# Kernel optimization log

Hardware: AMD Instinct MI355X
Metric: run time of the kernel (lower is better)

## Reference

```python
import jax, jax.numpy as jnp
import numpy as np

DILATIONS = (1, 2, 4, 8, 16, 32)
T_ENC = 168   # encoder context length
T_PRED = 24   # predict_sequence_length
FILTERS = 64
FEAT = 15
HIDDEN = 128
B = 2048


def setup_inputs() -> dict:
    key = jax.random.key(0)
    ks = jax.random.split(key, 12)
    w = lambda k, s: jax.random.normal(k, s, jnp.float32) * 0.05
    return {
        "decoder_features": jax.random.normal(ks[0], (B, T_PRED, FEAT), jnp.float32),
        "decoder_init_input": jax.random.normal(ks[1], (B, 1), jnp.float32),
        "encoder_outputs": jax.random.normal(ks[2], (len(DILATIONS), B, T_ENC, FILTERS), jnp.float32),
        "W1": w(ks[3], (FEAT + 1, FILTERS)), "b1": jnp.zeros((FILTERS,), jnp.float32),
        "W2": w(ks[4], (FILTERS, 2 * FILTERS)), "b2": jnp.zeros((2 * FILTERS,), jnp.float32),
        "W3": w(ks[5], (FILTERS, 2 * FILTERS)),
        "W4": w(ks[6], (FILTERS, 2 * FILTERS)), "b4": jnp.zeros((2 * FILTERS,), jnp.float32),
        "W5": w(ks[7], (FILTERS * len(DILATIONS), HIDDEN)), "b5": jnp.zeros((HIDDEN,), jnp.float32),
        "W6": w(ks[8], (HIDDEN, 1)), "b6": jnp.zeros((1,), jnp.float32),
    }


def reference(decoder_features, decoder_init_input, encoder_outputs,
              W1, b1, W2, b2, W3, W4, b4, W5, b5, W6, b6):
    L, Bd, Te, F = encoder_outputs.shape
    # Preallocated growing state buffer (the torch/keras code does tf.concat each step)
    bufs0 = jnp.concatenate(
        [encoder_outputs, jnp.zeros((L, Bd, T_PRED, F), encoder_outputs.dtype)], axis=2)

    def step(bufs, t):
        # Note: the source never updates prev_output, so (eval mode) this_input
        # always uses decoder_init_input concatenated with step-t features.
        this_input = jnp.concatenate(
            [decoder_init_input, decoder_features[:, t]], axis=-1)  # [B, FEAT+1]
        x = jnp.tanh(this_input @ W1 + b1)  # [B, F]
        skips_all = []
        for l, d in enumerate(DILATIONS):
            # encoder_outputs[l][:, -d, :] of a buffer of current length T_ENC + t
            state = jax.lax.dynamic_index_in_dim(
                bufs[l], T_ENC + t - d, axis=1, keepdims=False)  # [B, F]
            dc = state @ W2 + b2 + x @ W3  # [B, 2F]
            f, g = jnp.split(dc, 2, axis=1)
            gated = jnp.tanh(f) * jax.nn.sigmoid(g)  # [B, F]
            out = gated @ W4 + b4  # [B, 2F]
            skips, res = jnp.split(out, 2, axis=1)
            x = x + res
            bufs = bufs.at[l, :, T_ENC + t, :].set(x)
            skips_all.append(skips)
        sk = jax.nn.relu(jnp.concatenate(skips_all, axis=1))  # [B, F*L]
        h = jax.nn.relu(sk @ W5 + b5)  # [B, HIDDEN]
        y = h @ W6 + b6  # [B, 1]
        return bufs, y

    _, ys = jax.lax.scan(step, bufs0, jnp.arange(T_PRED))
    return jnp.transpose(ys, (1, 0, 2))  # [B, T_PRED, 1]
```

## Files before the change

kernel.cpp:

```cpp
#include <hip/hip_runtime.h>
#include <hip/hip_bf16.h>
#include <cstddef>

#define NB 2048
#define TENC 168
#define TPRED 24

typedef _Float16 h8 __attribute__((ext_vector_type(8)));
typedef float f4v __attribute__((ext_vector_type(4)));

#define LBAR() asm volatile("s_waitcnt lgkmcnt(0)\ns_barrier" ::: "memory")

__device__ __forceinline__ float tanh_fast(float v) {
  v = fminf(v, 15.0f);
  const float ex = __expf(2.0f * v);
  return (ex - 1.0f) * __builtin_amdgcn_rcpf(ex + 1.0f);
}
__device__ __forceinline__ float sig_fast(float v) {
  return __builtin_amdgcn_rcpf(1.0f + __expf(-v));
}

#define MFMA16(a, b, c) __builtin_amdgcn_mfma_f32_16x16x32_f16((a), (b), (c), 0, 0, 0)

__global__ __launch_bounds__(512, 1) void dec_phase1(
    const float* __restrict__ feat,
    const float* __restrict__ dinit,
    const float* __restrict__ enc,
    const float* __restrict__ W1,
    const float* __restrict__ b1,
    const float* __restrict__ W2,
    const float* __restrict__ b2,
    const float* __restrict__ W3,
    const float* __restrict__ W4,
    const float* __restrict__ b4,
    _Float16* __restrict__ skbuf,
    int t_steps)
{
  __shared__ _Float16 ring[23][16][72];
  __shared__ _Float16 g16v[2][16][72];
  __shared__ _Float16 xf16[16][72];
  __shared__ float    xf32[64][20];
  __shared__ _Float16 W43h[64][136];

  const int tid = threadIdx.x;
  const int w   = tid >> 6;
  const int ln  = tid & 63;
  const int i   = ln & 15;
  const int q   = ln >> 4;
  const int q8  = q * 8;
  const int e0  = blockIdx.x * 16;

  float* W3s  = (float*)&ring[0][0][0];
  float* W4rs = W3s + 64 * 128;
  for (int idx = tid; idx < 2048; idx += 512)
    ((float4*)W3s)[idx] = ((const float4*)W3)[idx];
  for (int idx = tid; idx < 1024; idx += 512) {
    const int row = idx >> 4, seg = idx & 15;
    *(float4*)&W4rs[row * 64 + seg * 4] = *(const float4*)&W4[row * 128 + 64 + seg * 4];
  }
  __syncthreads();
  {
    const int c = tid & 127, k0 = (tid >> 7) << 4;
    float acc[16];
    #pragma unroll
    for (int r = 0; r < 16; ++r) acc[r] = 0.0f;
    for (int m = 0; m < 64; ++m) {
      const float w3v = W3s[m * 128 + c];
      #pragma unroll
      for (int r = 0; r < 16; ++r) acc[r] += W4rs[(k0 + r) * 64 + m] * w3v;
    }
    #pragma unroll
    for (int r = 0; r < 16; ++r) W43h[k0 + r][c] = (_Float16)acc[r];
  }
  __syncthreads();

  const int fs = w & 3;
  const int cf = 16 * fs + i;
  const int cg = 64 + cf;
  const int cs = 16 * (w - 4) + i;

  h8 BW2f[2], BW2g[2], BW3f[2], BW3g[2], B43f[2], B43g[2], B4s[2], B4r[2];
  float b2f = 0.f, b2g = 0.f, b4s_b = 0.f, b4r_b = 0.f;
  if (w < 4) {
    #pragma unroll
    for (int kk = 0; kk < 2; ++kk)
      #pragma unroll
      for (int j = 0; j < 8; ++j) {
        const int k = kk * 32 + q8 + j;
        BW2f[kk][j] = (_Float16)W2[k * 128 + cf];
        BW2g[kk][j] = (_Float16)W2[k * 128 + cg];
        BW3f[kk][j] = (_Float16)W3[k * 128 + cf];
        BW3g[kk][j] = (_Float16)W3[k * 128 + cg];
        B43f[kk][j] = W43h[k][cf];
        B43g[kk][j] = W43h[k][cg];
      }
    b2f = b2[cf]; b2g = b2[cg];
  } else {
    #pragma unroll
    for (int kk = 0; kk < 2; ++kk)
      #pragma unroll
      for (int j = 0; j < 8; ++j) {
        const int k = kk * 32 + q8 + j;
        B4s[kk][j] = (_Float16)W4[k * 128 + cs];
        B4r[kk][j] = (_Float16)W4[k * 128 + 64 + cs];
      }
    b4s_b = b4[cs]; b4r_b = b4[64 + cs];
  }
  float w1r[16];
  #pragma unroll
  for (int ii = 0; ii < 16; ++ii) w1r[ii] = W1[ii * 64 + ln];
  const float b1r  = b1[ln];
  const float ini0 = dinit[e0 + 2 * w];
  const float ini1 = dinit[e0 + 2 * w + 1];

  for (int idx = tid; idx < 1920; idx += 512) {
    const int c = idx & 7, el = (idx >> 3) & 15, s = idx >> 7;
    int l, j;
    if (s == 0)      { l = 0; j = 0; }
    else if (s < 3)  { l = 1; j = s - 1; }
    else if (s < 7)  { l = 2; j = s - 3; }
    else             { l = 3; j = s - 7; }
    const int d = 1 << l;
    const float* ep = enc + (((size_t)l * NB + e0 + el) * TENC + (TENC + j - d)) * 64 + c * 8;
    h8 hv;
    #pragma unroll
    for (int u = 0; u < 8; ++u) hv[u] = (_Float16)ep[u];
    *(h8*)&ring[s][el][c * 8] = hv;
  }

  #pragma unroll
  for (int s = 0; s < 2; ++s) {
    const int el = 2 * w + s;
    const float* fp = feat + (size_t)(e0 + el) * TPRED * 15;
    float u = b1r + (s ? ini1 : ini0) * w1r[0];
    #pragma unroll
    for (int ii = 0; ii < 15; ++ii) u += fp[ii] * w1r[ii + 1];
    const float xv = tanh_fast(u);
    xf16[el][ln] = (_Float16)xv;
    xf32[ln][el] = xv;
  }
  LBAR();

  f4v Zf = {0,0,0,0}, Zg = {0,0,0,0}, xreg = {0,0,0,0};

  for (int t = 0; t < t_steps; ++t) {
    const int tn = (t + 1 < t_steps) ? t + 1 : t;
    f4v pfa[2], pfb[2], pfc[2];
    float2 pfd[2]; float pfe[2];
    #pragma unroll
    for (int s = 0; s < 2; ++s) {
      const float* fp = feat + ((size_t)(e0 + 2 * w + s) * TPRED + tn) * 15;
      pfa[s] = *(const f4v*)(fp);
      pfb[s] = *(const f4v*)(fp + 4);
      pfc[s] = *(const f4v*)(fp + 8);
      pfd[s] = *(const float2*)(fp + 12);
      pfe[s] = fp[14];
    }

    h8 s0a[4], s1a[4], s4a0, s4a1;
    f4v p4[4], p5[4];
    if (w < 4) {
      const int t4 = (t < 16) ? t : 0;
      const float* e4 = enc + (((size_t)4 * NB + e0 + i) * TENC + (152 + t4)) * 64 + q8;
      const float* e5 = enc + (((size_t)5 * NB + e0 + i) * TENC + (136 + t )) * 64 + q8;
      p4[0] = *(const f4v*)(e4);      p4[1] = *(const f4v*)(e4 + 4);
      p4[2] = *(const f4v*)(e4 + 32); p4[3] = *(const f4v*)(e4 + 36);
      p5[0] = *(const f4v*)(e5);      p5[1] = *(const f4v*)(e5 + 4);
      p5[2] = *(const f4v*)(e5 + 32); p5[3] = *(const f4v*)(e5 + 36);

      #pragma unroll
      for (int l = 0; l < 4; ++l) {
        const int d = 1 << l;
        const int slot = (d - 1) + (t & (d - 1));
        s0a[l] = *(const h8*)&ring[slot][i][q8];
        s1a[l] = *(const h8*)&ring[slot][i][32 + q8];
      }
      {
        const int slot4 = 15 + (t & 7);
        s4a0 = *(const h8*)&ring[slot4][i][q8];
        s4a1 = *(const h8*)&ring[slot4][i][32 + q8];
      }

      const h8 a2 = *(const h8*)&xf16[i][q8];
      const h8 a3 = *(const h8*)&xf16[i][32 + q8];
      Zf = (f4v){0,0,0,0};  Zg = (f4v){0,0,0,0};
      Zf = MFMA16(a2, BW3f[0], Zf); Zf = MFMA16(a3, BW3f[1], Zf);
      Zg = MFMA16(a2, BW3g[0], Zg); Zg = MFMA16(a3, BW3g[1], Zg);

      f4v dcf = Zf, dcg = Zg;
      dcf = MFMA16(s0a[0], BW2f[0], dcf); dcf = MFMA16(s1a[0], BW2f[1], dcf);
      dcg = MFMA16(s0a[0], BW2g[0], dcg); dcg = MFMA16(s1a[0], BW2g[1], dcg);
      #pragma unroll
      for (int r = 0; r < 4; ++r) {
        const float gd = tanh_fast(dcf[r] + b2f) * sig_fast(dcg[r] + b2g);
        g16v[0][4 * q + r][cf] = (_Float16)gd;
      }
    } else {
      xreg = *(const f4v*)&xf32[cs][4 * q];
    }
    LBAR();

    #pragma unroll
    for (int l = 1; l < 6; ++l) {
      const int pm1 = (l - 1) & 1;
      const h8 gA0 = *(const h8*)&g16v[pm1][i][q8];
      const h8 gA1 = *(const h8*)&g16v[pm1][i][32 + q8];

      if (w < 4) {
        Zf = MFMA16(gA0, B43f[0], Zf); Zf = MFMA16(gA1, B43f[1], Zf);
        Zg = MFMA16(gA0, B43g[0], Zg); Zg = MFMA16(gA1, B43g[1], Zg);
        h8 sa0, sa1;
        if (l <= 3) { sa0 = s0a[l]; sa1 = s1a[l]; }
        else if (l == 4) {
          if (t < 16) {
            #pragma unroll
            for (int u = 0; u < 4; ++u) {
              sa0[u] = (_Float16)p4[0][u]; sa0[u + 4] = (_Float16)p4[1][u];
              sa1[u] = (_Float16)p4[2][u]; sa1[u + 4] = (_Float16)p4[3][u];
            }
          } else { sa0 = s4a0; sa1 = s4a1; }
        } else {
          #pragma unroll
          for (int u = 0; u < 4; ++u) {
            sa0[u] = (_Float16)p5[0][u]; sa0[u + 4] = (_Float16)p5[1][u];
            sa1[u] = (_Float16)p5[2][u]; sa1[u + 4] = (_Float16)p5[3][u];
          }
        }
        f4v dcf = Zf, dcg = Zg;
        dcf = MFMA16(sa0, BW2f[0], dcf); dcf = MFMA16(sa1, BW2f[1], dcf);
        dcg = MFMA16(sa0, BW2g[0], dcg); dcg = MFMA16(sa1, BW2g[1], dcg);
        #pragma unroll
        for (int r = 0; r < 4; ++r) {
          const float gd = tanh_fast(dcf[r] + b2f) * sig_fast(dcg[r] + b2g);
          g16v[l & 1][4 * q + r][cf] = (_Float16)gd;
        }
      } else {
        const int lp  = l - 1;
        const int dlp = 1 << lp;
        const int slotlp = (lp <= 3) ? (dlp - 1) + (t & (dlp - 1)) : 15 + (t & 7);
        f4v osk = {0,0,0,0}, ore = {0,0,0,0};
        osk = MFMA16(gA0, B4s[0], osk); osk = MFMA16(gA1, B4s[1], osk);
        ore = MFMA16(gA0, B4r[0], ore); ore = MFMA16(gA1, B4r[1], ore);
        const bool wr = (t + dlp) <= 23;
        #pragma unroll
        for (int r = 0; r < 4; ++r) {
          skbuf[((size_t)(e0 + 4 * q + r) * TPRED + t) * 384 + lp * 64 + cs] =
              (_Float16)fmaxf(osk[r] + b4s_b, 0.0f);
          const float xn = xreg[r] + ore[r] + b4r_b;
          xreg[r] = xn;
          if (wr) ring[slotlp][4 * q + r][cs] = (_Float16)xn;
        }
      }
      LBAR();
    }

    if (w >= 4) {
      const h8 gA0 = *(const h8*)&g16v[1][i][q8];
      const h8 gA1 = *(const h8*)&g16v[1][i][32 + q8];
      f4v osk = {0,0,0,0};
      osk = MFMA16(gA0, B4s[0], osk); osk = MFMA16(gA1, B4s[1], osk);
      #pragma unroll
      for (int r = 0; r < 4; ++r)
        skbuf[((size_t)(e0 + 4 * q + r) * TPRED + t) * 384 + 5 * 64 + cs] =
            (_Float16)fmaxf(osk[r] + b4s_b, 0.0f);
    }
    if (t + 1 < t_steps) {
      #pragma unroll
      for (int s = 0; s < 2; ++s) {
        const int el = 2 * w + s;
        float u = b1r + (s ? ini1 : ini0) * w1r[0];
        u += pfa[s][0] * w1r[1]  + pfa[s][1] * w1r[2]  + pfa[s][2] * w1r[3]  + pfa[s][3] * w1r[4];
        u += pfb[s][0] * w1r[5]  + pfb[s][1] * w1r[6]  + pfb[s][2] * w1r[7]  + pfb[s][3] * w1r[8];
        u += pfc[s][0] * w1r[9]  + pfc[s][1] * w1r[10] + pfc[s][2] * w1r[11] + pfc[s][3] * w1r[12];
        u += pfd[s].x  * w1r[13] + pfd[s].y  * w1r[14] + pfe[s]    * w1r[15];
        const float xv = tanh_fast(u);
        xf16[el][ln] = (_Float16)xv;
        xf32[ln][el] = xv;
      }
    }
    LBAR();
  }
}

__global__ __launch_bounds__(512, 1) void dec_phase2(
    const _Float16* __restrict__ skbuf,
    const float* __restrict__ W5,
    const float* __restrict__ b5,
    const float* __restrict__ W6,
    const float* __restrict__ b6,
    float* __restrict__ out)
{
  __shared__ _Float16 As[192][392];
  __shared__ float red[192][8];

  const int tid = threadIdx.x;
  const int w   = tid >> 6;
  const int ln  = tid & 63;
  const int i   = ln & 15;
  const int q   = ln >> 4;
  const int R0  = blockIdx.x * 192;
  const int col = 16 * w + i;

  h8 B5[12];
  #pragma unroll
  for (int kk = 0; kk < 12; ++kk)
    #pragma unroll
    for (int j = 0; j < 8; ++j)
      B5[kk][j] = (_Float16)W5[(size_t)(kk * 32 + q * 8 + j) * 128 + col];
  const float b5r = b5[col], w6r = W6[col];

  h8 v1[9], v2[9];
  #pragma unroll
  for (int it = 0; it < 9; ++it) {
    const int idx = tid + it * 512;
    v1[it] = *(const h8*)&skbuf[(size_t)(R0 + idx / 48) * 384 + (idx % 48) * 8];
  }
  #pragma unroll
  for (int it = 0; it < 9; ++it) {
    const int idx = 4608 + tid + it * 512;
    v2[it] = *(const h8*)&skbuf[(size_t)(R0 + idx / 48) * 384 + (idx % 48) * 8];
  }
  #pragma unroll
  for (int it = 0; it < 9; ++it) {
    const int idx = tid + it * 512;
    *(h8*)&As[idx / 48][(idx % 48) * 8] = v1[it];
  }
  __syncthreads();
  #pragma unroll
  for (int it = 0; it < 9; ++it) {
    const int idx = 4608 + tid + it * 512;
    *(h8*)&As[idx / 48][(idx % 48) * 8] = v2[it];
  }

  #pragma unroll
  for (int m = 0; m < 12; ++m) {
    if (m == 6) __syncthreads();
    f4v acc = {0,0,0,0};
    #pragma unroll
    for (int kk = 0; kk < 12; ++kk) {
      const h8 a = *(const h8*)&As[16 * m + i][kk * 32 + q * 8];
      acc = MFMA16(a, B5[kk], acc);
    }
    float py[4];
    #pragma unroll
    for (int r = 0; r < 4; ++r)
      py[r] = fmaxf(acc[r] + b5r, 0.0f) * w6r;
    #pragma unroll
    for (int r = 0; r < 4; ++r) {
      float v = py[r];
      v += __shfl_xor(v, 1);
      v += __shfl_xor(v, 2);
      v += __shfl_xor(v, 4);
      v += __shfl_xor(v, 8);
      py[r] = v;
    }
    if (i == 0) {
      #pragma unroll
      for (int r = 0; r < 4; ++r) red[16 * m + 4 * q + r][w] = py[r];
    }
  }
  __syncthreads();

  if (tid < 192) {
    const f4v r0 = *(const f4v*)&red[tid][0];
    const f4v r1 = *(const f4v*)&red[tid][4];
    out[R0 + tid] = b6[0] + r0[0] + r0[1] + r0[2] + r0[3]
                          + r1[0] + r1[1] + r1[2] + r1[3];
  }
}

extern "C" void kernel_launch(void* const* d_in, const int* in_sizes, int n_in,
                              void* d_out, int out_size, void* d_ws, size_t ws_size,
                              hipStream_t stream) {
  const float* feat  = (const float*)d_in[0];
  const float* dinit = (const float*)d_in[1];
  const float* enc   = (const float*)d_in[2];
  const float* W1    = (const float*)d_in[3];
  const float* b1    = (const float*)d_in[4];
  const float* W2    = (const float*)d_in[5];
  const float* b2    = (const float*)d_in[6];
  const float* W3    = (const float*)d_in[7];
  const float* W4    = (const float*)d_in[8];
  const float* b4    = (const float*)d_in[9];
  const float* W5    = (const float*)d_in[10];
  const float* b5    = (const float*)d_in[11];
  const float* W6    = (const float*)d_in[12];
  const float* b6    = (const float*)d_in[13];

  float*     out   = (float*)d_out;
  _Float16*  skbuf = (_Float16*)d_ws;

  dec_phase1<<<dim3(128), dim3(512), 0, stream>>>(
      feat, dinit, enc, W1, b1, W2, b2, W3, W4, b4, skbuf, TPRED);
  dec_phase2<<<dim3(256), dim3(512), 0, stream>>>(
      skbuf, W5, b5, W6, b6, out);
}
```

Baseline: 117.7 us.

## Remove per-step barrier by overlapping W1 input projection and last skip with layer loop

Phase1 drops the separate end-of-step barrier. The next step's input projection (feature loads and tanh) moves onto the skip/residual waves during layers 3 and 5, using double-buffered xf16/xf32. The layer-5 skip output is deferred to the next step's layer 0. Biases are folded into MFMA accumulators, tanh*sigmoid is fused into one reciprocal using exp2, and gate waves get raised priority. Phase2 uses half-size tiles on twice as many blocks, which raises parallelism but reloads W5 per block more often.

```diff
diff --git a/kernel.cpp b/kernel.cpp
--- a/kernel.cpp
+++ b/kernel.cpp
@@ -9,18 +9,20 @@
 typedef _Float16 h8 __attribute__((ext_vector_type(8)));
 typedef float f4v __attribute__((ext_vector_type(4)));
 
+#define MFMA16(a, b, c) __builtin_amdgcn_mfma_f32_16x16x32_f16((a), (b), (c), 0, 0, 0)
+
 #define LBAR() asm volatile("s_waitcnt lgkmcnt(0)\ns_barrier" ::: "memory")
 
-__device__ __forceinline__ float tanh_fast(float v) {
-  v = fminf(v, 15.0f);
-  const float ex = __expf(2.0f * v);
-  return (ex - 1.0f) * __builtin_amdgcn_rcpf(ex + 1.0f);
+__device__ __forceinline__ float gate_fast(float a, float g) {
+  a = fminf(a, 15.0f);
+  const float e2a = __builtin_amdgcn_exp2f(a * 2.88539008177793f);
+  const float eg  = __builtin_amdgcn_exp2f(g * -1.44269504088896f);
+  return (e2a - 1.0f) * __builtin_amdgcn_rcpf((e2a + 1.0f) * (1.0f + eg));
 }
-__device__ __forceinline__ float sig_fast(float v) {
-  return __builtin_amdgcn_rcpf(1.0f + __expf(-v));
+__device__ __forceinline__ float tanh_fast(float u) {
+  const float e2 = __builtin_amdgcn_exp2f(fminf(u, 15.0f) * 2.88539008177793f);
+  return (e2 - 1.0f) * __builtin_amdgcn_rcpf(e2 + 1.0f);
 }
-
-#define MFMA16(a, b, c) __builtin_amdgcn_mfma_f32_16x16x32_f16((a), (b), (c), 0, 0, 0)
 
 __global__ __launch_bounds__(512, 1) void dec_phase1(
     const float* __restrict__ feat,
@@ -38,8 +40,8 @@
 {
   __shared__ _Float16 ring[23][16][72];
   __shared__ _Float16 g16v[2][16][72];
-  __shared__ _Float16 xf16[16][72];
-  __shared__ float    xf32[64][20];
+  __shared__ _Float16 xf16[2][16][72];
+  __shared__ float    xf32[2][64][20];
   __shared__ _Float16 W43h[64][136];
 
   const int tid = threadIdx.x;
@@ -77,10 +79,12 @@
   const int fs = w & 3;
   const int cf = 16 * fs + i;
   const int cg = 64 + cf;
-  const int cs = 16 * (w - 4) + i;
+  const int cw = w - 4;
+  const int cs = 16 * cw + i;
 
   h8 BW2f[2], BW2g[2], BW3f[2], BW3g[2], B43f[2], B43g[2], B4s[2], B4r[2];
   float b2f = 0.f, b2g = 0.f, b4s_b = 0.f, b4r_b = 0.f;
+  float w1r[16]; float b1r = 0.f; float ini4[4] = {0.f, 0.f, 0.f, 0.f};
   if (w < 4) {
     #pragma unroll
     for (int kk = 0; kk < 2; ++kk)
@@ -105,13 +109,12 @@
         B4r[kk][j] = (_Float16)W4[k * 128 + 64 + cs];
       }
     b4s_b = b4[cs]; b4r_b = b4[64 + cs];
-  }
-  float w1r[16];
-  #pragma unroll
-  for (int ii = 0; ii < 16; ++ii) w1r[ii] = W1[ii * 64 + ln];
-  const float b1r  = b1[ln];
-  const float ini0 = dinit[e0 + 2 * w];
-  const float ini1 = dinit[e0 + 2 * w + 1];
+    #pragma unroll
+    for (int ii = 0; ii < 16; ++ii) w1r[ii] = W1[ii * 64 + ln];
+    b1r = b1[ln];
+    #pragma unroll
+    for (int s2 = 0; s2 < 4; ++s2) ini4[s2] = dinit[e0 + 4 * cw + s2];
+  }
 
   for (int idx = tid; idx < 1920; idx += 512) {
     const int c = idx & 7, el = (idx >> 3) & 15, s = idx >> 7;
@@ -128,157 +131,177 @@
     *(h8*)&ring[s][el][c * 8] = hv;
   }
 
-  #pragma unroll
-  for (int s = 0; s < 2; ++s) {
-    const int el = 2 * w + s;
-    const float* fp = feat + (size_t)(e0 + el) * TPRED * 15;
-    float u = b1r + (s ? ini1 : ini0) * w1r[0];
-    #pragma unroll
-    for (int ii = 0; ii < 15; ++ii) u += fp[ii] * w1r[ii + 1];
-    const float xv = tanh_fast(u);
-    xf16[el][ln] = (_Float16)xv;
-    xf32[ln][el] = xv;
-  }
-  LBAR();
-
-  f4v Zf = {0,0,0,0}, Zg = {0,0,0,0}, xreg = {0,0,0,0};
+  {
+    float w1e[16];
+    #pragma unroll
+    for (int ii = 0; ii < 16; ++ii) w1e[ii] = W1[ii * 64 + ln];
+    const float b1e = b1[ln];
+    #pragma unroll
+    for (int s = 0; s < 2; ++s) {
+      const int el = 2 * w + s;
+      const float* fp = feat + (size_t)(e0 + el) * TPRED * 15;
+      float u = b1e + dinit[e0 + el] * w1e[0];
+      #pragma unroll
+      for (int ii = 0; ii < 15; ++ii) u += fp[ii] * w1e[ii + 1];
+      const float xv = tanh_fast(u);
+      xf16[0][el][ln] = (_Float16)xv;
+      xf32[0][ln][el] = xv;
+    }
+  }
+  __syncthreads();
+  if (w < 4) __builtin_amdgcn_s_setprio(1);
+
+  f4v Zf = {0,0,0,0}, Zg = {0,0,0,0};
 
   for (int t = 0; t < t_steps; ++t) {
-    const int tn = (t + 1 < t_steps) ? t + 1 : t;
-    f4v pfa[2], pfb[2], pfc[2];
-    float2 pfd[2]; float pfe[2];
-    #pragma unroll
-    for (int s = 0; s < 2; ++s) {
-      const float* fp = feat + ((size_t)(e0 + 2 * w + s) * TPRED + tn) * 15;
-      pfa[s] = *(const f4v*)(fp);
-      pfb[s] = *(const f4v*)(fp + 4);
-      pfc[s] = *(const f4v*)(fp + 8);
-      pfd[s] = *(const float2*)(fp + 12);
-      pfe[s] = fp[14];
-    }
-
     h8 s0a[4], s1a[4], s4a0, s4a1;
     f4v p4[4], p5[4];
-    if (w < 4) {
-      const int t4 = (t < 16) ? t : 0;
-      const float* e4 = enc + (((size_t)4 * NB + e0 + i) * TENC + (152 + t4)) * 64 + q8;
-      const float* e5 = enc + (((size_t)5 * NB + e0 + i) * TENC + (136 + t )) * 64 + q8;
-      p4[0] = *(const f4v*)(e4);      p4[1] = *(const f4v*)(e4 + 4);
-      p4[2] = *(const f4v*)(e4 + 32); p4[3] = *(const f4v*)(e4 + 36);
-      p5[0] = *(const f4v*)(e5);      p5[1] = *(const f4v*)(e5 + 4);
-      p5[2] = *(const f4v*)(e5 + 32); p5[3] = *(const f4v*)(e5 + 36);
-
-      #pragma unroll
-      for (int l = 0; l < 4; ++l) {
-        const int d = 1 << l;
-        const int slot = (d - 1) + (t & (d - 1));
-        s0a[l] = *(const h8*)&ring[slot][i][q8];
-        s1a[l] = *(const h8*)&ring[slot][i][32 + q8];
-      }
-      {
-        const int slot4 = 15 + (t & 7);
-        s4a0 = *(const h8*)&ring[slot4][i][q8];
-        s4a1 = *(const h8*)&ring[slot4][i][32 + q8];
-      }
-
-      const h8 a2 = *(const h8*)&xf16[i][q8];
-      const h8 a3 = *(const h8*)&xf16[i][32 + q8];
-      Zf = (f4v){0,0,0,0};  Zg = (f4v){0,0,0,0};
-      Zf = MFMA16(a2, BW3f[0], Zf); Zf = MFMA16(a3, BW3f[1], Zf);
-      Zg = MFMA16(a2, BW3g[0], Zg); Zg = MFMA16(a3, BW3g[1], Zg);
-
-      f4v dcf = Zf, dcg = Zg;
-      dcf = MFMA16(s0a[0], BW2f[0], dcf); dcf = MFMA16(s1a[0], BW2f[1], dcf);
-      dcg = MFMA16(s0a[0], BW2g[0], dcg); dcg = MFMA16(s1a[0], BW2g[1], dcg);
-      #pragma unroll
-      for (int r = 0; r < 4; ++r) {
-        const float gd = tanh_fast(dcf[r] + b2f) * sig_fast(dcg[r] + b2g);
-        g16v[0][4 * q + r][cf] = (_Float16)gd;
-      }
-    } else {
-      xreg = *(const f4v*)&xf32[cs][4 * q];
-    }
-    LBAR();
-
-    #pragma unroll
-    for (int l = 1; l < 6; ++l) {
-      const int pm1 = (l - 1) & 1;
-      const h8 gA0 = *(const h8*)&g16v[pm1][i][q8];
-      const h8 gA1 = *(const h8*)&g16v[pm1][i][32 + q8];
-
+    f4v ff0[4], ff1[4], ff2[4];
+    float2 ffd[4]; float ffe[4];
+    f4v xreg = {0,0,0,0};
+
+    for (int l = 0; l < 6; ++l) {
       if (w < 4) {
-        Zf = MFMA16(gA0, B43f[0], Zf); Zf = MFMA16(gA1, B43f[1], Zf);
-        Zg = MFMA16(gA0, B43g[0], Zg); Zg = MFMA16(gA1, B43g[1], Zg);
-        h8 sa0, sa1;
-        if (l <= 3) { sa0 = s0a[l]; sa1 = s1a[l]; }
-        else if (l == 4) {
-          if (t < 16) {
+        if (l == 0) {
+          const int t4 = (t < 16) ? t : 0;
+          const float* e4 = enc + (((size_t)4 * NB + e0 + i) * TENC + (152 + t4)) * 64 + q8;
+          const float* e5 = enc + (((size_t)5 * NB + e0 + i) * TENC + (136 + t )) * 64 + q8;
+          p4[0] = *(const f4v*)(e4);      p4[1] = *(const f4v*)(e4 + 4);
+          p4[2] = *(const f4v*)(e4 + 32); p4[3] = *(const f4v*)(e4 + 36);
+          p5[0] = *(const f4v*)(e5);      p5[1] = *(const f4v*)(e5 + 4);
+          p5[2] = *(const f4v*)(e5 + 32); p5[3] = *(const f4v*)(e5 + 36);
+
+          #pragma unroll
+          for (int ll = 0; ll < 4; ++ll) {
+            const int d = 1 << ll;
+            const int slot = (d - 1) + (t & (d - 1));
+            s0a[ll] = *(const h8*)&ring[slot][i][q8];
+            s1a[ll] = *(const h8*)&ring[slot][i][32 + q8];
+          }
+          {
+            const int slot4 = 15 + (t & 7);
+            s4a0 = *(const h8*)&ring[slot4][i][q8];
+            s4a1 = *(const h8*)&ring[slot4][i][32 + q8];
+          }
+
+          const h8 a2 = *(const h8*)&xf16[t & 1][i][q8];
+          const h8 a3 = *(const h8*)&xf16[t & 1][i][32 + q8];
+          Zf = (f4v){0,0,0,0};  Zg = (f4v){0,0,0,0};
+          Zf = MFMA16(a2, BW3f[0], Zf); Zf = MFMA16(a3, BW3f[1], Zf);
+          Zg = MFMA16(a2, BW3g[0], Zg); Zg = MFMA16(a3, BW3g[1], Zg);
+
+          f4v Sf = {b2f, b2f, b2f, b2f}, Sg = {b2g, b2g, b2g, b2g};
+          Sf = MFMA16(s0a[0], BW2f[0], Sf); Sf = MFMA16(s1a[0], BW2f[1], Sf);
+          Sg = MFMA16(s0a[0], BW2g[0], Sg); Sg = MFMA16(s1a[0], BW2g[1], Sg);
+          #pragma unroll
+          for (int r = 0; r < 4; ++r) {
+            const float gd = gate_fast(Zf[r] + Sf[r], Zg[r] + Sg[r]);
+            g16v[0][4 * q + r][cf] = (_Float16)gd;
+          }
+        } else {
+          const h8 gA0 = *(const h8*)&g16v[(l - 1) & 1][i][q8];
+          const h8 gA1 = *(const h8*)&g16v[(l - 1) & 1][i][32 + q8];
+          Zf = MFMA16(gA0, B43f[0], Zf); Zf = MFMA16(gA1, B43f[1], Zf);
+          Zg = MFMA16(gA0, B43g[0], Zg); Zg = MFMA16(gA1, B43g[1], Zg);
+          h8 sa0, sa1;
+          if (l <= 3) { sa0 = s0a[l]; sa1 = s1a[l]; }
+          else if (l == 4) {
+            if (t < 16) {
+              #pragma unroll
+              for (int u = 0; u < 4; ++u) {
+                sa0[u] = (_Float16)p4[0][u]; sa0[u + 4] = (_Float16)p4[1][u];
+                sa1[u] = (_Float16)p4[2][u]; sa1[u + 4] = (_Float16)p4[3][u];
+              }
+            } else { sa0 = s4a0; sa1 = s4a1; }
+          } else {
             #pragma unroll
             for (int u = 0; u < 4; ++u) {
-              sa0[u] = (_Float16)p4[0][u]; sa0[u + 4] = (_Float16)p4[1][u];
-              sa1[u] = (_Float16)p4[2][u]; sa1[u + 4] = (_Float16)p4[3][u];
+              sa0[u] = (_Float16)p5[0][u]; sa0[u + 4] = (_Float16)p5[1][u];
+              sa1[u] = (_Float16)p5[2][u]; sa1[u + 4] = (_Float16)p5[3][u];
             }
-          } else { sa0 = s4a0; sa1 = s4a1; }
-        } else {
-          #pragma unroll
-          for (int u = 0; u < 4; ++u) {
-            sa0[u] = (_Float16)p5[0][u]; sa0[u + 4] = (_Float16)p5[1][u];
-            sa1[u] = (_Float16)p5[2][u]; sa1[u + 4] = (_Float16)p5[3][u];
-          }
-        }
-        f4v dcf = Zf, dcg = Zg;
-        dcf = MFMA16(sa0, BW2f[0], dcf); dcf = MFMA16(sa1, BW2f[1], dcf);
-        dcg = MFMA16(sa0, BW2g[0], dcg); dcg = MFMA16(sa1, BW2g[1], dcg);
-        #pragma unroll
-        for (int r = 0; r < 4; ++r) {
-          const float gd = tanh_fast(dcf[r] + b2f) * sig_fast(dcg[r] + b2g);
-          g16v[l & 1][4 * q + r][cf] = (_Float16)gd;
+          }
+          f4v Sf = {b2f, b2f, b2f, b2f}, Sg = {b2g, b2g, b2g, b2g};
+          Sf = MFMA16(sa0, BW2f[0], Sf); Sf = MFMA16(sa1, BW2f[1], Sf);
+          Sg = MFMA16(sa0, BW2g[0], Sg); Sg = MFMA16(sa1, BW2g[1], Sg);
+          #pragma unroll
+          for (int r = 0; r < 4; ++r) {
+            const float gd = gate_fast(Zf[r] + Sf[r], Zg[r] + Sg[r]);
+            g16v[l & 1][4 * q + r][cf] = (_Float16)gd;
+          }
         }
       } else {
-        const int lp  = l - 1;
-        const int dlp = 1 << lp;
-        const int slotlp = (lp <= 3) ? (dlp - 1) + (t & (dlp - 1)) : 15 + (t & 7);
-        f4v osk = {0,0,0,0}, ore = {0,0,0,0};
-        osk = MFMA16(gA0, B4s[0], osk); osk = MFMA16(gA1, B4s[1], osk);
-        ore = MFMA16(gA0, B4r[0], ore); ore = MFMA16(gA1, B4r[1], ore);
-        const bool wr = (t + dlp) <= 23;
-        #pragma unroll
-        for (int r = 0; r < 4; ++r) {
-          skbuf[((size_t)(e0 + 4 * q + r) * TPRED + t) * 384 + lp * 64 + cs] =
-              (_Float16)fmaxf(osk[r] + b4s_b, 0.0f);
-          const float xn = xreg[r] + ore[r] + b4r_b;
-          xreg[r] = xn;
-          if (wr) ring[slotlp][4 * q + r][cs] = (_Float16)xn;
+        if (l == 0) {
+          xreg = *(const f4v*)&xf32[t & 1][cs][4 * q];
+          if (t > 0) {
+            const h8 g0 = *(const h8*)&g16v[1][i][q8];
+            const h8 g1 = *(const h8*)&g16v[1][i][32 + q8];
+            f4v osk = {b4s_b, b4s_b, b4s_b, b4s_b};
+            osk = MFMA16(g0, B4s[0], osk); osk = MFMA16(g1, B4s[1], osk);
+            #pragma unroll
+            for (int r = 0; r < 4; ++r)
+              skbuf[((size_t)(e0 + 4 * q + r) * TPRED + (t - 1)) * 384 + 5 * 64 + cs] =
+                  (_Float16)fmaxf(osk[r], 0.0f);
+          }
+        } else {
+          const int lp  = l - 1;
+          const int dlp = 1 << lp;
+          const int slotlp = (lp <= 3) ? (dlp - 1) + (t & (dlp - 1)) : 15 + (t & 7);
+          const h8 g0 = *(const h8*)&g16v[(l - 1) & 1][i][q8];
+          const h8 g1 = *(const h8*)&g16v[(l - 1) & 1][i][32 + q8];
+          f4v osk = {b4s_b, b4s_b, b4s_b, b4s_b};
+          osk = MFMA16(g0, B4s[0], osk); osk = MFMA16(g1, B4s[1], osk);
+          f4v ore = {b4r_b, b4r_b, b4r_b, b4r_b};
+          ore = MFMA16(g0, B4r[0], ore); ore = MFMA16(g1, B4r[1], ore);
+          const bool wr = (t + dlp) <= 23;
+          #pragma unroll
+          for (int r = 0; r < 4; ++r) {
+            skbuf[((size_t)(e0 + 4 * q + r) * TPRED + t) * 384 + lp * 64 + cs] =
+                (_Float16)fmaxf(osk[r], 0.0f);
+            const float xn = xreg[r] + ore[r];
+            xreg[r] = xn;
+            if (wr) ring[slotlp][4 * q + r][cs] = (_Float16)xn;
+          }
+        }
+        if (l == 3 && t + 1 < t_steps) {
+          #pragma unroll
+          for (int s2 = 0; s2 < 4; ++s2) {
+            const float* fp = feat + ((size_t)(e0 + 4 * cw + s2) * TPRED + (t + 1)) * 15;
+            ff0[s2] = *(const f4v*)(fp);
+            ff1[s2] = *(const f4v*)(fp + 4);
+            ff2[s2] = *(const f4v*)(fp + 8);
+            ffd[s2] = *(const float2*)(fp + 12);
+            ffe[s2] = fp[14];
+          }
+        }
+        if (l == 5 && t + 1 < t_steps) {
+          #pragma unroll
+          for (int s2 = 0; s2 < 4; ++s2) {
+            const int el = 4 * cw + s2;
+            float u = b1r + ini4[s2] * w1r[0];
+            u += ff0[s2][0] * w1r[1]  + ff0[s2][1] * w1r[2]  + ff0[s2][2] * w1r[3]  + ff0[s2][3] * w1r[4];
+            u += ff1[s2][0] * w1r[5]  + ff1[s2][1] * w1r[6]  + ff1[s2][2] * w1r[7]  + ff1[s2][3] * w1r[8];
+            u += ff2[s2][0] * w1r[9]  + ff2[s2][1] * w1r[10] + ff2[s2][2] * w1r[11] + ff2[s2][3] * w1r[12];
+            u += ffd[s2].x  * w1r[13] + ffd[s2].y  * w1r[14] + ffe[s2]    * w1r[15];
+            const float xv = tanh_fast(u);
+            xf16[(t + 1) & 1][el][ln] = (_Float16)xv;
+            xf32[(t + 1) & 1][ln][el] = xv;
+          }
         }
       }
       LBAR();
     }
-
-    if (w >= 4) {
-      const h8 gA0 = *(const h8*)&g16v[1][i][q8];
-      const h8 gA1 = *(const h8*)&g16v[1][i][32 + q8];
-      f4v osk = {0,0,0,0};
-      osk = MFMA16(gA0, B4s[0], osk); osk = MFMA16(gA1, B4s[1], osk);
-      #pragma unroll
-      for (int r = 0; r < 4; ++r)
-        skbuf[((size_t)(e0 + 4 * q + r) * TPRED + t) * 384 + 5 * 64 + cs] =
-            (_Float16)fmaxf(osk[r] + b4s_b, 0.0f);
-    }
-    if (t + 1 < t_steps) {
-      #pragma unroll
-      for (int s = 0; s < 2; ++s) {
-        const int el = 2 * w + s;
-        float u = b1r + (s ? ini1 : ini0) * w1r[0];
-        u += pfa[s][0] * w1r[1]  + pfa[s][1] * w1r[2]  + pfa[s][2] * w1r[3]  + pfa[s][3] * w1r[4];
-        u += pfb[s][0] * w1r[5]  + pfb[s][1] * w1r[6]  + pfb[s][2] * w1r[7]  + pfb[s][3] * w1r[8];
-        u += pfc[s][0] * w1r[9]  + pfc[s][1] * w1r[10] + pfc[s][2] * w1r[11] + pfc[s][3] * w1r[12];
-        u += pfd[s].x  * w1r[13] + pfd[s].y  * w1r[14] + pfe[s]    * w1r[15];
-        const float xv = tanh_fast(u);
-        xf16[el][ln] = (_Float16)xv;
-        xf32[ln][el] = xv;
-      }
-    }
-    LBAR();
+  }
+
+  if (w >= 4) {
+    const int s = t_steps - 1;
+    const h8 g0 = *(const h8*)&g16v[1][i][q8];
+    const h8 g1 = *(const h8*)&g16v[1][i][32 + q8];
+    f4v osk = {b4s_b, b4s_b, b4s_b, b4s_b};
+    osk = MFMA16(g0, B4s[0], osk); osk = MFMA16(g1, B4s[1], osk);
+    #pragma unroll
+    for (int r = 0; r < 4; ++r)
+      skbuf[((size_t)(e0 + 4 * q + r) * TPRED + s) * 384 + 5 * 64 + cs] =
+          (_Float16)fmaxf(osk[r], 0.0f);
   }
 }
 
@@ -290,15 +313,15 @@
     const float* __restrict__ b6,
     float* __restrict__ out)
 {
-  __shared__ _Float16 As[192][392];
-  __shared__ float red[192][8];
+  __shared__ _Float16 As[96][392];
+  __shared__ float red[96][8];
 
   const int tid = threadIdx.x;
   const int w   = tid >> 6;
   const int ln  = tid & 63;
   const int i   = ln & 15;
   const int q   = ln >> 4;
-  const int R0  = blockIdx.x * 192;
+  const int R0  = blockIdx.x * 96;
   const int col = 16 * w + i;
 
   h8 B5[12];
@@ -309,33 +332,17 @@
       B5[kk][j] = (_Float16)W5[(size_t)(kk * 32 + q * 8 + j) * 128 + col];
   const float b5r = b5[col], w6r = W6[col];
 
-  h8 v1[9], v2[9];
   #pragma unroll
   for (int it = 0; it < 9; ++it) {
     const int idx = tid + it * 512;
-    v1[it] = *(const h8*)&skbuf[(size_t)(R0 + idx / 48) * 384 + (idx % 48) * 8];
-  }
+    const h8 v = *(const h8*)&skbuf[(size_t)(R0 + idx / 48) * 384 + (idx % 48) * 8];
+    *(h8*)&As[idx / 48][(idx % 48) * 8] = v;
+  }
+  __syncthreads();
+
   #pragma unroll
-  for (int it = 0; it < 9; ++it) {
-    const int idx = 4608 + tid + it * 512;
-    v2[it] = *(const h8*)&skbuf[(size_t)(R0 + idx / 48) * 384 + (idx % 48) * 8];
-  }
-  #pragma unroll
-  for (int it = 0; it < 9; ++it) {
-    const int idx = tid + it * 512;
-    *(h8*)&As[idx / 48][(idx % 48) * 8] = v1[it];
-  }
-  __syncthreads();
-  #pragma unroll
-  for (int it = 0; it < 9; ++it) {
-    const int idx = 4608 + tid + it * 512;
-    *(h8*)&As[idx / 48][(idx % 48) * 8] = v2[it];
-  }
-
-  #pragma unroll
-  for (int m = 0; m < 12; ++m) {
-    if (m == 6) __syncthreads();
-    f4v acc = {0,0,0,0};
+  for (int m = 0; m < 6; ++m) {
+    f4v acc = {0, 0, 0, 0};
     #pragma unroll
     for (int kk = 0; kk < 12; ++kk) {
       const h8 a = *(const h8*)&As[16 * m + i][kk * 32 + q * 8];
@@ -361,7 +368,7 @@
   }
   __syncthreads();
 
-  if (tid < 192) {
+  if (tid < 96) {
     const f4v r0 = *(const f4v*)&red[tid][0];
     const f4v r1 = *(const f4v*)&red[tid][4];
     out[R0 + tid] = b6[0] + r0[0] + r0[1] + r0[2] + r0[3]
@@ -392,6 +399,6 @@
 
   dec_phase1<<<dim3(128), dim3(512), 0, stream>>>(
       feat, dinit, enc, W1, b1, W2, b2, W3, W4, b4, skbuf, TPRED);
-  dec_phase2<<<dim3(256), dim3(512), 0, stream>>>(
+  dec_phase2<<<dim3(512), dim3(512), 0, stream>>>(
       skbuf, W5, b5, W6, b6, out);
 }
```

Result: slower. 152.4 us, median of 2 (+29.5%).
